# Kernel tuning notes

Measured on AMD Instinct MI355X. Metric: run time of the kernel, lower is better.

## Reference

```python
import jax, jax.numpy as jnp
import numpy as np

B, C, T = 32, 512, 2048
OUT_SEQ_LEN = 80
SIGMA2 = 10.0


def setup_inputs() -> dict:
    key = jax.random.key(0)
    k1, k2, k3, k4, k5, k6 = jax.random.split(key, 6)
    x = jax.random.normal(k1, (B, C, T), dtype=jnp.float32)
    # lengths in [T//2, T], with at least one equal to T (torch broadcast assumes max(len)==T)
    len_fea = jax.random.randint(k2, (B,), T // 2, T + 1)
    len_fea = len_fea.at[0].set(T)
    s1 = 1.0 / np.sqrt(C)
    conv1_w = jax.random.uniform(k3, (C, C), jnp.float32, -s1, s1)   # 1x1 conv == linear [out,in]
    conv1_b = jax.random.uniform(k4, (C,), jnp.float32, -s1, s1)
    conv2_w = jax.random.uniform(k5, (C,), jnp.float32, -s1, s1)     # out_channels=1, squeezed
    conv2_b = jax.random.uniform(k6, (), jnp.float32, -s1, s1)
    return {"x": x, "len_fea": len_fea, "conv1_w": conv1_w, "conv1_b": conv1_b,
            "conv2_w": conv2_w, "conv2_b": conv2_b}


def reference(x, len_fea, conv1_w, conv1_b, conv2_w, conv2_b):
    b_size, _, Tt = x.shape
    unaligned = x  # [B,C,T]
    h = jax.nn.relu(x)
    h = jnp.einsum('oc,bct->bot', conv1_w, h) + conv1_b[None, :, None]  # 1x1 conv
    h = jax.nn.relu(h)
    g = jnp.einsum('c,bct->bt', conv2_w, h) + conv2_b                   # 1x1 conv to 1 channel
    g = jax.nn.sigmoid(g)                                               # rec=True path
    gls_ends = jnp.cumsum(g, axis=1)            # [B,T]
    gls_centers = gls_ends - g * 0.5            # [B,T]
    aligned_lengths = gls_ends[jnp.arange(b_size), len_fea - 1]         # [B]
    out_pos = 0.5 + jnp.arange(OUT_SEQ_LEN, dtype=x.dtype)              # rec=True positions
    w = gls_centers[:, None, :] - out_pos[None, :, None]                # [B,L,T]
    w = -(w * w) / SIGMA2
    mask = (jnp.arange(Tt)[None, :] >= len_fea[:, None]).astype(x.dtype)  # [B,T]
    w = w - 1e9 * mask[:, None, :]
    w = jax.nn.softmax(w, axis=-1)
    aligned_features = jnp.einsum('blt,bct->blc', w, unaligned)         # [B,L,C]
    return aligned_features, aligned_lengths
```

## Files before the change

### kernel.cpp

```cpp
#include <hip/hip_runtime.h>
#include <hip/hip_bf16.h>

#define NB 32
#define NC 512
#define NT 2048
#define NL 80
static constexpr float kInvSigma2 = 0.1f;

typedef __attribute__((ext_vector_type(8))) __bf16 bf16x8;
typedef __attribute__((ext_vector_type(4))) float f32x4;

__global__ __launch_bounds__(256) void k_w1p(const float* __restrict__ w1,
                                             __hip_bfloat16* __restrict__ w1p) {
  const int q = blockIdx.x * 256 + threadIdx.x;
  const int c_lo = (q & 3) << 3;
  const int o_lo = (q >> 2) & 15;
  const int c5 = (q >> 6) & 15;
  const int o4 = q >> 10;
  const int o = (o4 << 4) + o_lo;
  const int c = (c5 << 5) + c_lo;
  const float4 p0 = *reinterpret_cast<const float4*>(&w1[o * NC + c]);
  const float4 p1 = *reinterpret_cast<const float4*>(&w1[o * NC + c + 4]);
  bf16x8 v;
  v[0] = (__bf16)p0.x; v[1] = (__bf16)p0.y;
  v[2] = (__bf16)p0.z; v[3] = (__bf16)p0.w;
  v[4] = (__bf16)p1.x; v[5] = (__bf16)p1.y;
  v[6] = (__bf16)p1.z; v[7] = (__bf16)p1.w;
  *reinterpret_cast<bf16x8*>(&w1p[(size_t)q * 8]) = v;
}

__global__ __launch_bounds__(512, 4) void k_g_mfma(
    const float* __restrict__ x, const __hip_bfloat16* __restrict__ w1p,
    const float* __restrict__ b1, const float* __restrict__ w2,
    const float* __restrict__ b2, float* __restrict__ g) {
  __shared__ __hip_bfloat16 bs[64 * 512];
  __shared__ float pws[8][64];
  const int blk = blockIdx.x;
  const int b = blk >> 5;
  const int t0 = (blk & 31) << 6;
  const int tid = threadIdx.x;
  const int w = tid >> 6;
  const int lane = tid & 63;
  const int ln = tid & 15;
  const int kg = lane >> 4;
  const int ob = w << 6;

  {
    const int tl = (tid & 15) << 2;
    const int cp = (tid >> 4) << 1;
    const float* xb = x + (size_t)b * NC * NT + t0;
#pragma unroll
    for (int i = 0; i < 8; ++i) {
      const int c = (i << 6) + cp;
      const float4 va =
          *reinterpret_cast<const float4*>(&xb[(size_t)c * NT + tl]);
      const float4 vb =
          *reinterpret_cast<const float4*>(&xb[(size_t)(c + 1) * NT + tl]);
      const float fa[4] = {va.x, va.y, va.z, va.w};
      const float fb[4] = {vb.x, vb.y, vb.z, vb.w};
#pragma unroll
      for (int j = 0; j < 4; ++j) {
        const int t = tl + j;
        const __hip_bfloat16 lo = __float2bfloat16(fmaxf(fa[j], 0.f));
        const __hip_bfloat16 hi = __float2bfloat16(fmaxf(fb[j], 0.f));
        const unsigned pk =
            ((unsigned)*reinterpret_cast<const unsigned short*>(&hi) << 16) |
            *reinterpret_cast<const unsigned short*>(&lo);
        *reinterpret_cast<unsigned*>(
            (char*)bs + (t << 10) +
            ((((c >> 3) ^ (t & 7)) << 4) | ((c & 7) << 1))) = pk;
      }
    }
  }
  __syncthreads();

  f32x4 acc[4][4];
#pragma unroll
  for (int ot = 0; ot < 4; ++ot)
#pragma unroll
    for (int nt = 0; nt < 4; ++nt) acc[ot][nt] = (f32x4){0.f, 0.f, 0.f, 0.f};

  int rowb[4], xm[4];
#pragma unroll
  for (int nt = 0; nt < 4; ++nt) {
    const int tr = (nt << 4) + ln;
    rowb[nt] = tr << 10;
    xm[nt] = (tr & 7) << 4;
  }
  const __hip_bfloat16* abase =
      w1p + ((size_t)w << 15) + (ln << 5) + (kg << 3);
  const char* bsb = (const char*)bs;

#pragma unroll 4
  for (int ks = 0; ks < 16; ++ks) {
    const int gb = (ks << 6) + (kg << 4);
    bf16x8 bfrag[4];
#pragma unroll
    for (int nt = 0; nt < 4; ++nt)
      bfrag[nt] = *reinterpret_cast<const bf16x8*>(
          bsb + rowb[nt] + (gb ^ xm[nt]));
#pragma unroll
    for (int ot = 0; ot < 4; ++ot) {
      const bf16x8 af = *reinterpret_cast<const bf16x8*>(
          abase + (ot << 13) + (ks << 9));
#pragma unroll
      for (int nt = 0; nt < 4; ++nt)
        acc[ot][nt] = __builtin_amdgcn_mfma_f32_16x16x32_bf16(
            af, bfrag[nt], acc[ot][nt], 0, 0, 0);
    }
  }

  float pl[4] = {0.f, 0.f, 0.f, 0.f};
#pragma unroll
  for (int ot = 0; ot < 4; ++ot) {
    const int o4 = ob + (ot << 4) + (kg << 2);
    const float4 b1v = *reinterpret_cast<const float4*>(&b1[o4]);
    const float4 w2v = *reinterpret_cast<const float4*>(&w2[o4]);
#pragma unroll
    for (int nt = 0; nt < 4; ++nt) {
      pl[nt] = fmaf(w2v.x, fmaxf(acc[ot][nt][0] + b1v.x, 0.f), pl[nt]);
      pl[nt] = fmaf(w2v.y, fmaxf(acc[ot][nt][1] + b1v.y, 0.f), pl[nt]);
      pl[nt] = fmaf(w2v.z, fmaxf(acc[ot][nt][2] + b1v.z, 0.f), pl[nt]);
      pl[nt] = fmaf(w2v.w, fmaxf(acc[ot][nt][3] + b1v.w, 0.f), pl[nt]);
    }
  }
#pragma unroll
  for (int nt = 0; nt < 4; ++nt) {
    pl[nt] += __shfl_xor(pl[nt], 16, 64);
    pl[nt] += __shfl_xor(pl[nt], 32, 64);
  }
  if (kg == 0) {
#pragma unroll
    for (int nt = 0; nt < 4; ++nt) pws[w][(nt << 4) + ln] = pl[nt];
  }
  __syncthreads();
  if (tid < 64) {
    float s = b2[0];
#pragma unroll
    for (int i = 0; i < 8; ++i) s += pws[i][tid];
    g[b * NT + t0 + tid] = 1.f / (1.f + __expf(-s));
  }
}

__global__ __launch_bounds__(256) void k_g_slow(const float* __restrict__ x,
                                                const float* __restrict__ w1,
                                                const float* __restrict__ b1,
                                                const float* __restrict__ w2,
                                                const float* __restrict__ b2,
                                                float* __restrict__ g) {
  __shared__ __hip_bfloat16 xs[NC][64];
  const int blk = blockIdx.x;
  const int b = blk >> 5;
  const int t0 = (blk & 31) << 6;
  const int tid = threadIdx.x;
  {
    const int tl = (tid & 15) << 2;
    const int c0 = tid >> 4;
    for (int c = c0; c < NC; c += 16) {
      const float4 v = *reinterpret_cast<const float4*>(
          &x[((size_t)b * NC + c) * NT + t0 + tl]);
      xs[c][tl + 0] = __float2bfloat16(fmaxf(v.x, 0.f));
      xs[c][tl + 1] = __float2bfloat16(fmaxf(v.y, 0.f));
      xs[c][tl + 2] = __float2bfloat16(fmaxf(v.z, 0.f));
      xs[c][tl + 3] = __float2bfloat16(fmaxf(v.w, 0.f));
    }
  }
  __syncthreads();
  const int og = tid >> 6;
  const int t = tid & 63;
  float gacc = 0.f;
  for (int pass = 0; pass < 16; ++pass) {
    const int o0 = (og << 7) + (pass << 3);
    float h[8];
#pragma unroll
    for (int j = 0; j < 8; ++j) h[j] = b1[o0 + j];
    const float* wrow = w1 + (size_t)o0 * NC;
#pragma unroll 4
    for (int c = 0; c < NC; ++c) {
      const float xv = __bfloat162float(xs[c][t]);
#pragma unroll
      for (int j = 0; j < 8; ++j) h[j] = fmaf(wrow[j * NC + c], xv, h[j]);
    }
    float p = 0.f;
#pragma unroll
    for (int j = 0; j < 8; ++j) p = fmaf(w2[o0 + j], fmaxf(h[j], 0.f), p);
    gacc += p;
  }
  __syncthreads();
  float* gr = reinterpret_cast<float*>(&xs[0][0]);
  gr[og * 64 + t] = gacc;
  __syncthreads();
  if (tid < 64) {
    const float s = gr[tid] + gr[64 + tid] + gr[128 + tid] + gr[192 + tid] + b2[0];
    g[b * NT + t0 + tid] = 1.f / (1.f + __expf(-s));
  }
}

__global__ __launch_bounds__(256) void k_scan(const float* __restrict__ g,
                                              const int* __restrict__ len_fea,
                                              float* __restrict__ centers,
                                              float* __restrict__ out_len) {
  const int b = blockIdx.x;
  const int tid = threadIdx.x;
  const float* gb = g + b * NT;
  float v[8];
  {
    const float4 p0 = *reinterpret_cast<const float4*>(&gb[tid * 8]);
    const float4 p1 = *reinterpret_cast<const float4*>(&gb[tid * 8 + 4]);
    v[0] = p0.x; v[1] = p0.y; v[2] = p0.z; v[3] = p0.w;
    v[4] = p1.x; v[5] = p1.y; v[6] = p1.z; v[7] = p1.w;
  }
  float s = 0.f;
#pragma unroll
  for (int j = 0; j < 8; ++j) s += v[j];
  float wscan = s;
  const int lane = tid & 63, wid = tid >> 6;
#pragma unroll
  for (int off = 1; off < 64; off <<= 1) {
    const float o = __shfl_up(wscan, (unsigned)off, 64);
    if (lane >= off) wscan += o;
  }
  __shared__ float wsum[4];
  if (lane == 63) wsum[wid] = wscan;
  __syncthreads();
  float base = 0.f;
#pragma unroll
  for (int i = 0; i < 4; ++i)
    if (i < wid) base += wsum[i];
  float run = base + wscan - s;
  const int li = len_fea[b] - 1;
#pragma unroll
  for (int j = 0; j < 8; ++j) {
    const int t = tid * 8 + j;
    run += v[j];
    centers[b * NT + t] = run - 0.5f * v[j];
    if (t == li) out_len[b] = run;
  }
}

__global__ __launch_bounds__(256) void k_wstats(
    const float* __restrict__ centers, const int* __restrict__ len_fea,
    __hip_bfloat16* __restrict__ wbf) {
  const int b = blockIdx.x / NL;
  const int l = blockIdx.x % NL;
  const int tid = threadIdx.x;
  const int len = len_fea[b];
  const float pos = 0.5f + (float)l;
  const float* cb = centers + b * NT;
  const int t0 = tid * 8;

  float cv[8];
  {
    const float4 p0 = *reinterpret_cast<const float4*>(&cb[t0]);
    const float4 p1 = *reinterpret_cast<const float4*>(&cb[t0 + 4]);
    cv[0] = p0.x; cv[1] = p0.y; cv[2] = p0.z; cv[3] = p0.w;
    cv[4] = p1.x; cv[5] = p1.y; cv[6] = p1.z; cv[7] = p1.w;
  }
  float lg[8];
  float m = -3.0e38f;
#pragma unroll
  for (int j = 0; j < 8; ++j) {
    if (t0 + j < len) {
      const float d = cv[j] - pos;
      lg[j] = -d * d * kInvSigma2;
      m = fmaxf(m, lg[j]);
    } else {
      lg[j] = -3.0e38f;
    }
  }
  const int lane = tid & 63, wid = tid >> 6;
#pragma unroll
  for (int off = 32; off > 0; off >>= 1) m = fmaxf(m, __shfl_xor(m, off, 64));
  __shared__ float redm[4];
  if (lane == 0) redm[wid] = m;
  __syncthreads();
  const float M = fmaxf(fmaxf(redm[0], redm[1]), fmaxf(redm[2], redm[3]));

  float e[8];
  float ssum = 0.f;
#pragma unroll
  for (int j = 0; j < 8; ++j) {
    e[j] = (t0 + j < len) ? __expf(lg[j] - M) : 0.f;
    ssum += e[j];
  }
#pragma unroll
  for (int off = 32; off > 0; off >>= 1) ssum += __shfl_xor(ssum, off, 64);
  __shared__ float reds[4];
  if (lane == 0) reds[wid] = ssum;
  __syncthreads();
  const float rinv = 1.f / (reds[0] + reds[1] + reds[2] + reds[3]);

  bf16x8 o;
#pragma unroll
  for (int j = 0; j < 8; ++j) o[j] = (__bf16)(e[j] * rinv);
  *reinterpret_cast<bf16x8*>(&wbf[((size_t)b * NL + l) * NT + t0]) = o;
}

__global__ __launch_bounds__(256) void k_out_mfma(
    const float* __restrict__ x, const __hip_bfloat16* __restrict__ wbf,
    float* __restrict__ out) {
  __shared__ float red[3][64][41];
  const int blk = blockIdx.x;
  const int b = blk >> 4;
  const int c0 = (blk & 15) << 5;
  const int tid = threadIdx.x;
  const int w = tid >> 6;
  const int lane = tid & 63;
  const int ln = tid & 15;
  const int kg = lane >> 4;
  const int tbase = w << 9;

  f32x4 acc[5][2];
#pragma unroll
  for (int lt = 0; lt < 5; ++lt)
#pragma unroll
    for (int nt = 0; nt < 2; ++nt) acc[lt][nt] = (f32x4){0.f, 0.f, 0.f, 0.f};

  const __hip_bfloat16* abase =
      wbf + ((size_t)b * NL + ln) * NT + tbase + (kg << 3);
  const float* bbase = x + ((size_t)b * NC + c0 + ln) * NT + tbase + (kg << 3);

#pragma unroll 4
  for (int ks = 0; ks < 16; ++ks) {
    const int ck = ks << 5;
    bf16x8 bfrag[2];
#pragma unroll
    for (int nt = 0; nt < 2; ++nt) {
      const float4 p0 =
          *reinterpret_cast<const float4*>(bbase + nt * 16 * NT + ck);
      const float4 p1 =
          *reinterpret_cast<const float4*>(bbase + nt * 16 * NT + ck + 4);
      bf16x8 v;
      v[0] = (__bf16)p0.x; v[1] = (__bf16)p0.y;
      v[2] = (__bf16)p0.z; v[3] = (__bf16)p0.w;
      v[4] = (__bf16)p1.x; v[5] = (__bf16)p1.y;
      v[6] = (__bf16)p1.z; v[7] = (__bf16)p1.w;
      bfrag[nt] = v;
    }
#pragma unroll
    for (int lt = 0; lt < 5; ++lt) {
      const bf16x8 af =
          *reinterpret_cast<const bf16x8*>(abase + lt * 16 * NT + ck);
      acc[lt][0] = __builtin_amdgcn_mfma_f32_16x16x32_bf16(af, bfrag[0],
                                                           acc[lt][0], 0, 0, 0);
      acc[lt][1] = __builtin_amdgcn_mfma_f32_16x16x32_bf16(af, bfrag[1],
                                                           acc[lt][1], 0, 0, 0);
    }
  }

  if (w > 0) {
#pragma unroll
    for (int lt = 0; lt < 5; ++lt)
#pragma unroll
      for (int nt = 0; nt < 2; ++nt)
#pragma unroll
        for (int j = 0; j < 4; ++j)
          red[w - 1][lane][lt * 8 + nt * 4 + j] = acc[lt][nt][j];
  }
  __syncthreads();
  if (w == 0) {
#pragma unroll
    for (int lt = 0; lt < 5; ++lt)
#pragma unroll
      for (int nt = 0; nt < 2; ++nt)
#pragma unroll
        for (int j = 0; j < 4; ++j) {
          float s = acc[lt][nt][j];
#pragma unroll
          for (int i = 0; i < 3; ++i) s += red[i][lane][lt * 8 + nt * 4 + j];
          const int l = lt * 16 + (kg << 2) + j;
          out[((size_t)b * NL + l) * NC + c0 + nt * 16 + ln] = s;
        }
  }
}

__global__ __launch_bounds__(256) void k_stats(const float* __restrict__ centers,
                                               const int* __restrict__ len_fea,
                                               float* __restrict__ rmax,
                                               float* __restrict__ rinv) {
  const int b = blockIdx.x / NL;
  const int l = blockIdx.x % NL;
  const int tid = threadIdx.x;
  const int len = len_fea[b];
  const float pos = 0.5f + (float)l;
  const float* cb = centers + b * NT;
  float lg[8];
  float m = -3.0e38f;
  const int t0 = tid * 8;
#pragma unroll
  for (int j = 0; j < 8; ++j) {
    const int t = t0 + j;
    if (t < len) {
      const float d = cb[t] - pos;
      lg[j] = -d * d * kInvSigma2;
      m = fmaxf(m, lg[j]);
    } else {
      lg[j] = -3.0e38f;
    }
  }
  const int lane = tid & 63, wid = tid >> 6;
#pragma unroll
  for (int off = 32; off > 0; off >>= 1) m = fmaxf(m, __shfl_xor(m, off, 64));
  __shared__ float redm[4];
  if (lane == 0) redm[wid] = m;
  __syncthreads();
  const float M = fmaxf(fmaxf(redm[0], redm[1]), fmaxf(redm[2], redm[3]));
  float ssum = 0.f;
#pragma unroll
  for (int j = 0; j < 8; ++j) {
    if (t0 + j < len) ssum += __expf(lg[j] - M);
  }
#pragma unroll
  for (int off = 32; off > 0; off >>= 1) ssum += __shfl_xor(ssum, off, 64);
  __shared__ float reds[4];
  if (lane == 0) reds[wid] = ssum;
  __syncthreads();
  if (tid == 0) {
    const float S = reds[0] + reds[1] + reds[2] + reds[3];
    rmax[blockIdx.x] = M;
    rinv[blockIdx.x] = 1.f / S;
  }
}

__global__ __launch_bounds__(128) void k_out(const float* __restrict__ x,
                                             const int* __restrict__ len_fea,
                                             const float* __restrict__ centers,
                                             const float* __restrict__ rmax,
                                             const float* __restrict__ rinv,
                                             float* __restrict__ out) {
  __shared__ float xsh[128][65];
  __shared__ float wsh[20][64];
  const int blk = blockIdx.x;
  const int b = blk >> 4;
  const int l0 = ((blk >> 2) & 3) * 20;
  const int c0 = (blk & 3) * 128;
  const int tid = threadIdx.x;
  const int len = len_fea[b];
  float acc[20];
#pragma unroll
  for (int l = 0; l < 20; ++l) acc[l] = 0.f;

  for (int t0 = 0; t0 < NT; t0 += 64) {
    __syncthreads();
    {
      const int tl = (tid & 15) << 2;
      const int r0 = tid >> 4;
      for (int r = r0; r < 128; r += 8) {
        const float4 v = *reinterpret_cast<const float4*>(
            &x[((size_t)b * NC + c0 + r) * NT + t0 + tl]);
        float* p = &xsh[r][tl];
        p[0] = v.x; p[1] = v.y; p[2] = v.z; p[3] = v.w;
      }
    }
#pragma unroll
    for (int k = 0; k < 10; ++k) {
      const int idx = k * 128 + tid;
      const int l = idx >> 6;
      const int tt = idx & 63;
      float wv = 0.f;
      if (t0 + tt < len) {
        const float d = centers[b * NT + t0 + tt] - (0.5f + (float)(l0 + l));
        wv = __expf(-d * d * kInvSigma2 - rmax[b * NL + l0 + l]) *
             rinv[b * NL + l0 + l];
      }
      wsh[l][tt] = wv;
    }
    __syncthreads();
#pragma unroll 4
    for (int tt = 0; tt < 64; ++tt) {
      const float xv = xsh[tid][tt];
#pragma unroll
      for (int l = 0; l < 20; ++l) acc[l] = fmaf(wsh[l][tt], xv, acc[l]);
    }
  }
#pragma unroll
  for (int l = 0; l < 20; ++l)
    out[((size_t)b * NL + l0 + l) * NC + c0 + tid] = acc[l];
}

extern "C" void kernel_launch(void* const* d_in, const int* in_sizes, int n_in,
                              void* d_out, int out_size, void* d_ws, size_t ws_size,
                              hipStream_t stream) {
  const float* x = (const float*)d_in[0];
  const int* len_fea = (const int*)d_in[1];
  const float* w1 = (const float*)d_in[2];
  const float* b1 = (const float*)d_in[3];
  const float* w2 = (const float*)d_in[4];
  const float* b2 = (const float*)d_in[5];

  float* out = (float*)d_out;
  float* out_len = out + (size_t)NB * NL * NC;

  float* ws = (float*)d_ws;
  float* g = ws;
  float* centers = ws + NB * NT;
  float* rmax = ws + 2 * NB * NT;
  float* rinv = rmax + NB * NL;
  __hip_bfloat16* w1p = (__hip_bfloat16*)(rinv + NB * NL);
  __hip_bfloat16* wbf = w1p + (size_t)NC * NC;

  const size_t need_mid = (size_t)(2 * NB * NT + 2 * NB * NL) * 4 +
                          (size_t)NC * NC * 2;
  const size_t need_full = need_mid + (size_t)NB * NL * NT * 2;

  if (ws_size >= need_full) {
    k_w1p<<<(NC * NC) / 2048, 256, 0, stream>>>(w1, w1p);
    k_g_mfma<<<NB * 32, 512, 0, stream>>>(x, w1p, b1, w2, b2, g);
    k_scan<<<NB, 256, 0, stream>>>(g, len_fea, centers, out_len);
    k_wstats<<<NB * NL, 256, 0, stream>>>(centers, len_fea, wbf);
    k_out_mfma<<<NB * 16, 256, 0, stream>>>(x, wbf, out);
  } else if (ws_size >= need_mid) {
    k_w1p<<<(NC * NC) / 2048, 256, 0, stream>>>(w1, w1p);
    k_g_mfma<<<NB * 32, 512, 0, stream>>>(x, w1p, b1, w2, b2, g);
    k_scan<<<NB, 256, 0, stream>>>(g, len_fea, centers, out_len);
    k_stats<<<NB * NL, 256, 0, stream>>>(centers, len_fea, rmax, rinv);
    k_out<<<NB * 16, 128, 0, stream>>>(x, len_fea, centers, rmax, rinv, out);
  } else {
    k_g_slow<<<NB * 32, 256, 0, stream>>>(x, w1, b1, w2, b2, g);
    k_scan<<<NB, 256, 0, stream>>>(g, len_fea, centers, out_len);
    k_stats<<<NB * NL, 256, 0, stream>>>(centers, len_fea, rmax, rinv);
    k_out<<<NB * 16, 128, 0, stream>>>(x, len_fea, centers, rmax, rinv, out);
  }
}
```

Measured before the change: 104.6 us.

## Split x staging into two halves overlapped with MFMA k-loop, widen LDS swizzle

The x tile staging into LDS is split into two channel halves. The second half's global loads are issued before the first half of the MFMA k-loop, then converted and written to LDS after it, so load latency overlaps compute. The LDS XOR swizzle now also mixes in bits (t>>3), and s_setprio is raised around the MFMA block. Holding the second-half data in registers adds register pressure, which may reduce occupancy. Writing the second half while other waves may still be reading is safe only because the halves use disjoint channel ranges.

```diff
diff --git a/kernel.cpp b/kernel.cpp
--- a/kernel.cpp
+++ b/kernel.cpp
@@ -45,34 +45,42 @@
   const int kg = lane >> 4;
   const int ob = w << 6;
 
-  {
-    const int tl = (tid & 15) << 2;
-    const int cp = (tid >> 4) << 1;
-    const float* xb = x + (size_t)b * NC * NT + t0;
-#pragma unroll
-    for (int i = 0; i < 8; ++i) {
-      const int c = (i << 6) + cp;
-      const float4 va =
-          *reinterpret_cast<const float4*>(&xb[(size_t)c * NT + tl]);
-      const float4 vb =
-          *reinterpret_cast<const float4*>(&xb[(size_t)(c + 1) * NT + tl]);
-      const float fa[4] = {va.x, va.y, va.z, va.w};
-      const float fb[4] = {vb.x, vb.y, vb.z, vb.w};
-#pragma unroll
-      for (int j = 0; j < 4; ++j) {
-        const int t = tl + j;
-        const __hip_bfloat16 lo = __float2bfloat16(fmaxf(fa[j], 0.f));
-        const __hip_bfloat16 hi = __float2bfloat16(fmaxf(fb[j], 0.f));
-        const unsigned pk =
-            ((unsigned)*reinterpret_cast<const unsigned short*>(&hi) << 16) |
-            *reinterpret_cast<const unsigned short*>(&lo);
-        *reinterpret_cast<unsigned*>(
-            (char*)bs + (t << 10) +
-            ((((c >> 3) ^ (t & 7)) << 4) | ((c & 7) << 1))) = pk;
-      }
-    }
-  }
-  __syncthreads();
+  const int tl = (tid & 15) << 2;
+  const int cp = (tid >> 4) << 1;
+  const float* xb = x + (size_t)b * NC * NT + t0;
+
+  auto wr_pair = [&](int t, int c, float lo_f, float hi_f) {
+    const __hip_bfloat16 lo = __float2bfloat16(fmaxf(lo_f, 0.f));
+    const __hip_bfloat16 hi = __float2bfloat16(fmaxf(hi_f, 0.f));
+    const unsigned pk =
+        ((unsigned)*reinterpret_cast<const unsigned short*>(&hi) << 16) |
+        *reinterpret_cast<const unsigned short*>(&lo);
+    const int gran = ((c >> 3) ^ (t & 7) ^ ((t >> 3) & 7)) & 7;
+    const int base = (c >> 3) & ~7;
+    *reinterpret_cast<unsigned*>(
+        (char*)bs + (t << 10) + (((base | gran) << 4) | ((c & 7) << 1))) = pk;
+  };
+
+#pragma unroll
+  for (int i = 0; i < 4; ++i) {
+    const int c = (i << 6) + cp;
+    const float4 va = *reinterpret_cast<const float4*>(&xb[(size_t)c * NT + tl]);
+    const float4 vb =
+        *reinterpret_cast<const float4*>(&xb[(size_t)(c + 1) * NT + tl]);
+    const float fa[4] = {va.x, va.y, va.z, va.w};
+    const float fb[4] = {vb.x, vb.y, vb.z, vb.w};
+#pragma unroll
+    for (int j = 0; j < 4; ++j) wr_pair(tl + j, c, fa[j], fb[j]);
+  }
+  __syncthreads();
+
+  float4 ha[4], hb[4];
+#pragma unroll
+  for (int i = 0; i < 4; ++i) {
+    const int c = 256 + (i << 6) + cp;
+    ha[i] = *reinterpret_cast<const float4*>(&xb[(size_t)c * NT + tl]);
+    hb[i] = *reinterpret_cast<const float4*>(&xb[(size_t)(c + 1) * NT + tl]);
+  }
 
   f32x4 acc[4][4];
 #pragma unroll
@@ -85,30 +93,48 @@
   for (int nt = 0; nt < 4; ++nt) {
     const int tr = (nt << 4) + ln;
     rowb[nt] = tr << 10;
-    xm[nt] = (tr & 7) << 4;
+    xm[nt] = (((tr & 7) ^ ((tr >> 3) & 7)) & 7) << 4;
   }
   const __hip_bfloat16* abase =
       w1p + ((size_t)w << 15) + (ln << 5) + (kg << 3);
   const char* bsb = (const char*)bs;
 
+  auto kloop = [&](int ks0, int ks1) {
 #pragma unroll 4
-  for (int ks = 0; ks < 16; ++ks) {
-    const int gb = (ks << 6) + (kg << 4);
-    bf16x8 bfrag[4];
-#pragma unroll
-    for (int nt = 0; nt < 4; ++nt)
-      bfrag[nt] = *reinterpret_cast<const bf16x8*>(
-          bsb + rowb[nt] + (gb ^ xm[nt]));
-#pragma unroll
-    for (int ot = 0; ot < 4; ++ot) {
-      const bf16x8 af = *reinterpret_cast<const bf16x8*>(
-          abase + (ot << 13) + (ks << 9));
+    for (int ks = ks0; ks < ks1; ++ks) {
+      const int gb = (ks << 6) + (kg << 4);
+      bf16x8 bfrag[4];
 #pragma unroll
       for (int nt = 0; nt < 4; ++nt)
-        acc[ot][nt] = __builtin_amdgcn_mfma_f32_16x16x32_bf16(
-            af, bfrag[nt], acc[ot][nt], 0, 0, 0);
-    }
-  }
+        bfrag[nt] = *reinterpret_cast<const bf16x8*>(
+            bsb + rowb[nt] + (gb ^ xm[nt]));
+      __builtin_amdgcn_s_setprio(1);
+#pragma unroll
+      for (int ot = 0; ot < 4; ++ot) {
+        const bf16x8 af = *reinterpret_cast<const bf16x8*>(
+            abase + (ot << 13) + (ks << 9));
+#pragma unroll
+        for (int nt = 0; nt < 4; ++nt)
+          acc[ot][nt] = __builtin_amdgcn_mfma_f32_16x16x32_bf16(
+              af, bfrag[nt], acc[ot][nt], 0, 0, 0);
+      }
+      __builtin_amdgcn_s_setprio(0);
+    }
+  };
+
+  kloop(0, 8);
+
+#pragma unroll
+  for (int i = 0; i < 4; ++i) {
+    const int c = 256 + (i << 6) + cp;
+    const float fa[4] = {ha[i].x, ha[i].y, ha[i].z, ha[i].w};
+    const float fb[4] = {hb[i].x, hb[i].y, hb[i].z, hb[i].w};
+#pragma unroll
+    for (int j = 0; j < 4; ++j) wr_pair(tl + j, c, fa[j], fb[j]);
+  }
+  __syncthreads();
+
+  kloop(8, 16);
 
   float pl[4] = {0.f, 0.f, 0.f, 0.f};
 #pragma unroll
```

Measured after the change: 122.7 us. 17.4% more time.
